# Kernel optimization log

Measured on AMD Instinct MI355X. Metric: run time of the kernel, lower is better.

The kernel has to match this reference:

```python
import jax, jax.numpy as jnp
import numpy as np

P = 7       # patch (window) size
H_HEADS = 8
D_HEAD = 64
SCALE = D_HEAD ** -0.5


def setup_inputs() -> dict:
    key = jax.random.key(0)
    k1, k2, k3, k4 = jax.random.split(key, 4)
    dim, inner = 256, H_HEADS * D_HEAD
    fmap = jax.random.normal(k1, (32, 56, 56, dim), dtype=jnp.float32)
    Wq = jax.random.normal(k2, (dim, inner), dtype=jnp.float32) * (dim ** -0.5)
    Wkv = jax.random.normal(k3, (dim, 2 * inner), dtype=jnp.float32) * (dim ** -0.5)
    Wo = jax.random.normal(k4, (inner, dim), dtype=jnp.float32) * (inner ** -0.5)
    bo = jnp.zeros((dim,), dtype=jnp.float32)
    return {"fmap": fmap, "Wq": Wq, "Wkv": Wkv, "Wo": Wo, "bo": bo}


def reference(fmap, Wq, Wkv, Wo, bo):
    b, X, Y, c = fmap.shape
    x, y = X // P, Y // P
    h, d = H_HEADS, D_HEAD
    # window partition: b (x p1) (y p2) c -> (b x y) p1 p2 c
    f = fmap.reshape(b, x, P, y, P, c).transpose(0, 1, 3, 2, 4, 5)
    f = f.reshape(b * x * y, P, P, c)
    # 1x1 convs == matmul over channels
    q = f @ Wq                       # (B, p, p, h*d)
    k_, v = jnp.split(f @ Wkv, 2, axis=-1)
    B = b * x * y
    pp = P * P
    def to_heads(t):  # (B,p,p,h*d) -> (B,h,pp,d)
        return t.reshape(B, pp, h, d).transpose(0, 2, 1, 3)
    q, k_, v = map(to_heads, (q, k_, v))
    dots = jnp.einsum('bhid,bhjd->bhij', q, k_) * SCALE
    attn = jax.nn.softmax(dots, axis=-1)
    out = jnp.einsum('bhij,bhjd->bhid', attn, v)      # (B,h,pp,d)
    # (b x y h) (p1 p2) d -> b (x p1) (y p2) (h d)
    out = out.reshape(b, x, y, h, P, P, d)
    out = out.transpose(0, 1, 4, 2, 5, 3, 6).reshape(b, X, Y, h * d)
    return out @ Wo + bo
```

## Files before the change

kernel.cpp:

```cpp
#include <hip/hip_runtime.h>
#include <hip/hip_bf16.h>

typedef __bf16 bf16;
typedef __bf16 bf16x4 __attribute__((ext_vector_type(4)));
typedef __bf16 bf16x8 __attribute__((ext_vector_type(8)));
typedef float f32x4 __attribute__((ext_vector_type(4)));

#define TOK 100352
#define ATT_SCALE 0.125f

#define GLOAD_LDS16(g, l)                                                        \
  __builtin_amdgcn_global_load_lds((const __attribute__((address_space(1))) void*)(g), \
                                   (__attribute__((address_space(3))) void*)(l), 16, 0, 0)

__global__ __launch_bounds__(256) void transpose_cast_k(const float* __restrict__ in,
                                                        bf16* __restrict__ out, int R, int C) {
  __shared__ float t[32][33];
  int c0 = blockIdx.x * 32, r0 = blockIdx.y * 32;
  int tx = threadIdx.x, ty = threadIdx.y;
#pragma unroll
  for (int i = ty; i < 32; i += 8)
    t[i][tx] = in[(size_t)(r0 + i) * C + c0 + tx];
  __syncthreads();
#pragma unroll
  for (int i = ty; i < 32; i += 8)
    out[(size_t)(c0 + i) * R + r0 + tx] = (bf16)t[tx][i];
}

__global__ __launch_bounds__(256) void cast_partition_k(const float* __restrict__ fmap,
                                                        bf16* __restrict__ A, int tok0) {
  int tid = blockIdx.x * 256 + threadIdx.x;
  int tokl = tid >> 5, cg = (tid & 31) << 3;
  int tok = tok0 + tokl;
  int w = tok / 49, t = tok - w * 49;
  int p1 = t / 7, p2 = t - p1 * 7;
  int bb = w >> 6, xx = (w >> 3) & 7, yy = w & 7;
  size_t src = ((((size_t)bb * 56) + xx * 7 + p1) * 56 + yy * 7 + p2) * 256 + cg;
  float4 f0 = *(const float4*)(fmap + src);
  float4 f1 = *(const float4*)(fmap + src + 4);
  bf16x8 o;
  o[0] = (bf16)f0.x; o[1] = (bf16)f0.y; o[2] = (bf16)f0.z; o[3] = (bf16)f0.w;
  o[4] = (bf16)f1.x; o[5] = (bf16)f1.y; o[6] = (bf16)f1.z; o[7] = (bf16)f1.w;
  *(bf16x8*)(A + (size_t)tokl * 256 + cg) = o;
}

template <int KD, int ND, int EPI>
__global__ __launch_bounds__(256) void gemm_bt_k(const bf16* __restrict__ A,
                                                 const bf16* __restrict__ Bt,
                                                 bf16* __restrict__ Cb, float* __restrict__ Cf,
                                                 const float* __restrict__ bias, int tok0) {
  __shared__ bf16 As[128 * 64], Bs[128 * 64];
  const int tid = threadIdx.x;
  const int lane = tid & 63, wv = tid >> 6;
  const int l15 = lane & 15, l4 = lane >> 4;
  const int bn = blockIdx.x, bm = blockIdx.y;
  const int mb = (wv >> 1) * 64, nb = (wv & 1) * 64;
  const int srow = wv * 32 + (lane >> 3);
  const int scol = ((lane & 7) ^ ((lane >> 3) & 7)) * 8;
  const bf16* Ab = A + (size_t)(bm * 128 + srow) * KD + scol;
  const bf16* Bb = Bt + (size_t)(bn * 128 + srow) * KD + scol;
  f32x4 acc[4][4] = {};
  for (int ks = 0; ks < KD / 64; ++ks) {
#pragma unroll
    for (int i = 0; i < 4; ++i) {
      GLOAD_LDS16(Ab + (size_t)i * 8 * KD + ks * 64, As + wv * 2048 + i * 512);
      GLOAD_LDS16(Bb + (size_t)i * 8 * KD + ks * 64, Bs + wv * 2048 + i * 512);
    }
    __syncthreads();
#pragma unroll
    for (int kk = 0; kk < 2; ++kk) {
      bf16x8 af[4], bfr[4];
#pragma unroll
      for (int m = 0; m < 4; ++m) {
        int r = mb + m * 16 + l15;
        af[m] = *(const bf16x8*)((const char*)As +
                 ((r * 128 + kk * 64 + l4 * 16) ^ ((r & 7) << 4)));
      }
#pragma unroll
      for (int n = 0; n < 4; ++n) {
        int r = nb + n * 16 + l15;
        bfr[n] = *(const bf16x8*)((const char*)Bs +
                 ((r * 128 + kk * 64 + l4 * 16) ^ ((r & 7) << 4)));
      }
#pragma unroll
      for (int m = 0; m < 4; ++m)
#pragma unroll
        for (int n = 0; n < 4; ++n)
          acc[m][n] = __builtin_amdgcn_mfma_f32_16x16x32_bf16(bfr[n], af[m], acc[m][n], 0, 0, 0);
    }
    __syncthreads();
  }
  if constexpr (EPI == 1) {
#pragma unroll
    for (int m = 0; m < 4; ++m) {
      size_t row = (size_t)bm * 128 + mb + m * 16 + l15;
#pragma unroll
      for (int n = 0; n < 4; ++n) {
        int col = bn * 128 + nb + n * 16 + l4 * 4;
        bf16x4 pk;
#pragma unroll
        for (int r = 0; r < 4; ++r) pk[r] = (bf16)acc[m][n][r];
        *(bf16x4*)(Cb + row * ND + col) = pk;
      }
    }
  } else {
#pragma unroll
    for (int m = 0; m < 4; ++m) {
      int tok = tok0 + bm * 128 + mb + m * 16 + l15;
      int w = tok / 49, t = tok - w * 49;
      int p1 = t / 7, p2 = t - p1 * 7;
      int bb = w >> 6, xx = (w >> 3) & 7, yy = w & 7;
      size_t orow = (((size_t)bb * 56) + xx * 7 + p1) * 56 + yy * 7 + p2;
#pragma unroll
      for (int n = 0; n < 4; ++n) {
        int col = bn * 128 + nb + n * 16 + l4 * 4;
        float4 b4 = *(const float4*)(bias + col);
        float4 v;
        v.x = acc[m][n][0] + b4.x;
        v.y = acc[m][n][1] + b4.y;
        v.z = acc[m][n][2] + b4.z;
        v.w = acc[m][n][3] + b4.w;
        *(float4*)(Cf + orow * 256 + col) = v;
      }
    }
  }
}

__global__ __launch_bounds__(256) void attn_win_k(const bf16* __restrict__ qkv,
                                                  bf16* __restrict__ attn) {
  __shared__ bf16 Qs[64 * 64], Ks[64 * 64], Vt[64 * 64], Ps[4 * 16 * 64];
  int blk = blockIdx.x;
  int w = blk >> 3, h = blk & 7;
  int tid = threadIdx.x, lane = tid & 63, wv = tid >> 6;
  int l15 = lane & 15, l4 = lane >> 4;
  const size_t base = (size_t)w * 49 * 1536 + h * 64;
#pragma unroll
  for (int i = 0; i < 2; ++i) {
    int j = i * 256 + tid, r = j >> 3, cc = j & 7;
    int off = (r * 128 + cc * 16) ^ ((r & 7) << 4);
    uint4 zq = {0, 0, 0, 0}, zk = {0, 0, 0, 0};
    if (r < 49) {
      zq = *(const uint4*)(qkv + base + (size_t)r * 1536 + cc * 8);
      zk = *(const uint4*)(qkv + base + 512 + (size_t)r * 1536 + cc * 8);
    }
    *(uint4*)((char*)Qs + off) = zq;
    *(uint4*)((char*)Ks + off) = zk;
  }
#pragma unroll
  for (int i = 0; i < 2; ++i) {
    int j = i * 256 + tid, r = j >> 3, cg = j & 7;
    if (r < 49) {
      uint4 v = *(const uint4*)(qkv + base + 1024 + (size_t)r * 1536 + cg * 8);
      const bf16* pv = (const bf16*)&v;
#pragma unroll
      for (int e = 0; e < 8; ++e) {
        int c = cg * 8 + e;
        int off = ((c * 64 + r) * 2) ^ (((c >> 3) & 7) << 4);
        *(bf16*)((char*)Vt + off) = pv[e];
      }
    } else {
#pragma unroll
      for (int e = 0; e < 8; ++e) {
        int c = cg * 8 + e;
        int off = ((c * 64 + r) * 2) ^ (((c >> 3) & 7) << 4);
        *(bf16*)((char*)Vt + off) = (bf16)0.0f;
      }
    }
  }
  __syncthreads();
  f32x4 s[4] = {};
#pragma unroll
  for (int kk = 0; kk < 2; ++kk) {
    int rq = wv * 16 + l15;
    bf16x8 aq = *(const bf16x8*)((const char*)Qs +
                ((rq * 128 + kk * 64 + l4 * 16) ^ ((rq & 7) << 4)));
#pragma unroll
    for (int n = 0; n < 4; ++n) {
      int rk = n * 16 + l15;
      bf16x8 bk = *(const bf16x8*)((const char*)Ks +
                  ((rk * 128 + kk * 64 + l4 * 16) ^ ((rk & 7) << 4)));
      s[n] = __builtin_amdgcn_mfma_f32_16x16x32_bf16(aq, bk, s[n], 0, 0, 0);
    }
  }
  float pr[4][4];
#pragma unroll
  for (int reg = 0; reg < 4; ++reg) {
    float m = -1e30f;
#pragma unroll
    for (int n = 0; n < 4; ++n) {
      float v = s[n][reg] * ATT_SCALE;
      if (n * 16 + l15 < 49) m = fmaxf(m, v);
    }
#pragma unroll
    for (int d = 1; d < 16; d <<= 1) m = fmaxf(m, __shfl_xor(m, d));
    float sum = 0.f;
#pragma unroll
    for (int n = 0; n < 4; ++n) {
      float p = (n * 16 + l15 < 49) ? __expf(s[n][reg] * ATT_SCALE - m) : 0.f;
      pr[n][reg] = p;
      sum += p;
    }
#pragma unroll
    for (int d = 1; d < 16; d <<= 1) sum += __shfl_xor(sum, d);
    float inv = 1.f / sum;
#pragma unroll
    for (int n = 0; n < 4; ++n) pr[n][reg] *= inv;
  }
  char* pbase = (char*)Ps + wv * 2048;
#pragma unroll
  for (int n = 0; n < 4; ++n)
#pragma unroll
    for (int reg = 0; reg < 4; ++reg) {
      int rl = l4 * 4 + reg, col = n * 16 + l15;
      int off = ((rl * 64 + col) * 2) ^ ((rl & 7) << 4);
      *(bf16*)(pbase + off) = (bf16)pr[n][reg];
    }
  __syncthreads();
  f32x4 o[4] = {};
#pragma unroll
  for (int kk = 0; kk < 2; ++kk) {
    int rp = l15;
    bf16x8 ap = *(const bf16x8*)(pbase +
                ((rp * 128 + kk * 64 + l4 * 16) ^ ((rp & 7) << 4)));
#pragma unroll
    for (int n = 0; n < 4; ++n) {
      int rv = n * 16 + l15;
      bf16x8 bv = *(const bf16x8*)((const char*)Vt +
                  ((rv * 128 + kk * 64 + l4 * 16) ^ (((rv >> 3) & 7) << 4)));
      o[n] = __builtin_amdgcn_mfma_f32_16x16x32_bf16(bv, ap, o[n], 0, 0, 0);
    }
  }
  int rl = wv * 16 + l15;
  if (rl < 49) {
    size_t rowoff = ((size_t)w * 49 + rl) * 512 + h * 64;
#pragma unroll
    for (int n = 0; n < 4; ++n) {
      bf16x4 pk;
#pragma unroll
      for (int r = 0; r < 4; ++r) pk[r] = (bf16)o[n][r];
      *(bf16x4*)(attn + rowoff + n * 16 + l4 * 4) = pk;
    }
  }
}

extern "C" void kernel_launch(void* const* d_in, const int* in_sizes, int n_in,
                              void* d_out, int out_size, void* d_ws, size_t ws_size,
                              hipStream_t stream) {
  const float* fmap = (const float*)d_in[0];
  const float* Wq = (const float*)d_in[1];
  const float* Wkv = (const float*)d_in[2];
  const float* Wo = (const float*)d_in[3];
  const float* bo = (const float*)d_in[4];
  float* out = (float*)d_out;
  char* ws = (char*)d_ws;

  const size_t WQKV_B = 1536ull * 256 * 2;
  const size_t WO_B = 256ull * 512 * 2;
  const size_t wbytes = WQKV_B + WO_B;

  int nc = 0;
  size_t Tc = 0;
  for (int c = 1; c <= 16; c <<= 1) {
    size_t tc = TOK / c;
    if (wbytes + tc * 4608ull <= ws_size) { nc = c; Tc = tc; break; }
  }
  if (nc == 0) return;

  bf16* Wqkv_t = (bf16*)(ws);
  bf16* Wo_t = (bf16*)(ws + WQKV_B);
  bf16* Abuf = (bf16*)(ws + wbytes);
  bf16* qkv = (bf16*)(ws + wbytes + Tc * 512);
  bf16* attn = (bf16*)(ws + wbytes + Tc * 512 + Tc * 3072);

  hipLaunchKernelGGL(transpose_cast_k, dim3(16, 8), dim3(32, 8), 0, stream, Wq, Wqkv_t, 256, 512);
  hipLaunchKernelGGL(transpose_cast_k, dim3(32, 8), dim3(32, 8), 0, stream, Wkv,
                     Wqkv_t + 512 * 256, 256, 1024);
  hipLaunchKernelGGL(transpose_cast_k, dim3(8, 16), dim3(32, 8), 0, stream, Wo, Wo_t, 512, 256);

  for (int c = 0; c < nc; ++c) {
    int tok0 = (int)(c * Tc);
    int wloc = (int)(Tc / 49);
    hipLaunchKernelGGL(cast_partition_k, dim3((int)(Tc / 8)), dim3(256), 0, stream, fmap, Abuf,
                       tok0);
    hipLaunchKernelGGL((gemm_bt_k<256, 1536, 1>), dim3(12, (int)(Tc / 128)), dim3(256), 0, stream,
                       Abuf, Wqkv_t, qkv, nullptr, nullptr, 0);
    hipLaunchKernelGGL(attn_win_k, dim3(wloc * 8), dim3(256), 0, stream, qkv, attn);
    hipLaunchKernelGGL((gemm_bt_k<512, 256, 2>), dim3(2, (int)(Tc / 128)), dim3(256), 0, stream,
                       attn, Wo_t, nullptr, out, bo, tok0);
  }
}
```

Baseline: 366.5 us.

## Fuse window partition into QKV GEMM and output projection into attention

Result: slower. 426.1 us (+16.3%).

```diff
diff --git a/kernel.cpp b/kernel.cpp
--- a/kernel.cpp
+++ b/kernel.cpp
@@ -27,28 +27,9 @@
     out[(size_t)(c0 + i) * R + r0 + tx] = (bf16)t[tx][i];
 }
 
-__global__ __launch_bounds__(256) void cast_partition_k(const float* __restrict__ fmap,
-                                                        bf16* __restrict__ A, int tok0) {
-  int tid = blockIdx.x * 256 + threadIdx.x;
-  int tokl = tid >> 5, cg = (tid & 31) << 3;
-  int tok = tok0 + tokl;
-  int w = tok / 49, t = tok - w * 49;
-  int p1 = t / 7, p2 = t - p1 * 7;
-  int bb = w >> 6, xx = (w >> 3) & 7, yy = w & 7;
-  size_t src = ((((size_t)bb * 56) + xx * 7 + p1) * 56 + yy * 7 + p2) * 256 + cg;
-  float4 f0 = *(const float4*)(fmap + src);
-  float4 f1 = *(const float4*)(fmap + src + 4);
-  bf16x8 o;
-  o[0] = (bf16)f0.x; o[1] = (bf16)f0.y; o[2] = (bf16)f0.z; o[3] = (bf16)f0.w;
-  o[4] = (bf16)f1.x; o[5] = (bf16)f1.y; o[6] = (bf16)f1.z; o[7] = (bf16)f1.w;
-  *(bf16x8*)(A + (size_t)tokl * 256 + cg) = o;
-}
-
-template <int KD, int ND, int EPI>
-__global__ __launch_bounds__(256) void gemm_bt_k(const bf16* __restrict__ A,
-                                                 const bf16* __restrict__ Bt,
-                                                 bf16* __restrict__ Cb, float* __restrict__ Cf,
-                                                 const float* __restrict__ bias, int tok0) {
+__global__ __launch_bounds__(256) void qkv_gemm_k(const float* __restrict__ fmap,
+                                                  const bf16* __restrict__ Bt,
+                                                  bf16* __restrict__ Cb, int tok0) {
   __shared__ bf16 As[128 * 64], Bs[128 * 64];
   const int tid = threadIdx.x;
   const int lane = tid & 63, wv = tid >> 6;
@@ -57,14 +38,33 @@
   const int mb = (wv >> 1) * 64, nb = (wv & 1) * 64;
   const int srow = wv * 32 + (lane >> 3);
   const int scol = ((lane & 7) ^ ((lane >> 3) & 7)) * 8;
-  const bf16* Ab = A + (size_t)(bm * 128 + srow) * KD + scol;
-  const bf16* Bb = Bt + (size_t)(bn * 128 + srow) * KD + scol;
+  const bf16* Bb = Bt + (size_t)(bn * 128 + srow) * 256 + scol;
+  const int arow = tid >> 3;
+  const int acc8 = tid & 7;
+  int sro[4];
+#pragma unroll
+  for (int i = 0; i < 4; ++i) {
+    int tok = tok0 + bm * 128 + i * 32 + arow;
+    int w = tok / 49, t = tok - w * 49;
+    int p1 = t / 7, p2 = t - p1 * 7;
+    int bb = w >> 6, xx = (w >> 3) & 7, yy = w & 7;
+    sro[i] = ((bb * 56 + xx * 7 + p1) * 56 + yy * 7 + p2) * 256;
+  }
   f32x4 acc[4][4] = {};
-  for (int ks = 0; ks < KD / 64; ++ks) {
+  for (int ks = 0; ks < 4; ++ks) {
+#pragma unroll
+    for (int i = 0; i < 4; ++i)
+      GLOAD_LDS16(Bb + (size_t)i * 8 * 256 + ks * 64, Bs + wv * 2048 + i * 512);
 #pragma unroll
     for (int i = 0; i < 4; ++i) {
-      GLOAD_LDS16(Ab + (size_t)i * 8 * KD + ks * 64, As + wv * 2048 + i * 512);
-      GLOAD_LDS16(Bb + (size_t)i * 8 * KD + ks * 64, Bs + wv * 2048 + i * 512);
+      const float* p = fmap + sro[i] + ks * 64 + acc8 * 8;
+      float4 f0 = *(const float4*)p;
+      float4 f1 = *(const float4*)(p + 4);
+      bf16x8 o;
+      o[0] = (bf16)f0.x; o[1] = (bf16)f0.y; o[2] = (bf16)f0.z; o[3] = (bf16)f0.w;
+      o[4] = (bf16)f1.x; o[5] = (bf16)f1.y; o[6] = (bf16)f1.z; o[7] = (bf16)f1.w;
+      int r = i * 32 + arow;
+      *(bf16x8*)((char*)As + ((r * 128 + acc8 * 16) ^ ((r & 7) << 4))) = o;
     }
     __syncthreads();
 #pragma unroll
@@ -90,67 +90,51 @@
     }
     __syncthreads();
   }
-  if constexpr (EPI == 1) {
-#pragma unroll
-    for (int m = 0; m < 4; ++m) {
-      size_t row = (size_t)bm * 128 + mb + m * 16 + l15;
-#pragma unroll
-      for (int n = 0; n < 4; ++n) {
-        int col = bn * 128 + nb + n * 16 + l4 * 4;
-        bf16x4 pk;
-#pragma unroll
-        for (int r = 0; r < 4; ++r) pk[r] = (bf16)acc[m][n][r];
-        *(bf16x4*)(Cb + row * ND + col) = pk;
-      }
-    }
-  } else {
-#pragma unroll
-    for (int m = 0; m < 4; ++m) {
-      int tok = tok0 + bm * 128 + mb + m * 16 + l15;
-      int w = tok / 49, t = tok - w * 49;
-      int p1 = t / 7, p2 = t - p1 * 7;
-      int bb = w >> 6, xx = (w >> 3) & 7, yy = w & 7;
-      size_t orow = (((size_t)bb * 56) + xx * 7 + p1) * 56 + yy * 7 + p2;
-#pragma unroll
-      for (int n = 0; n < 4; ++n) {
-        int col = bn * 128 + nb + n * 16 + l4 * 4;
-        float4 b4 = *(const float4*)(bias + col);
-        float4 v;
-        v.x = acc[m][n][0] + b4.x;
-        v.y = acc[m][n][1] + b4.y;
-        v.z = acc[m][n][2] + b4.z;
-        v.w = acc[m][n][3] + b4.w;
-        *(float4*)(Cf + orow * 256 + col) = v;
-      }
+#pragma unroll
+  for (int m = 0; m < 4; ++m) {
+    size_t row = (size_t)bm * 128 + mb + m * 16 + l15;
+#pragma unroll
+    for (int n = 0; n < 4; ++n) {
+      int col = bn * 128 + nb + n * 16 + l4 * 4;
+      bf16x4 pk;
+#pragma unroll
+      for (int r = 0; r < 4; ++r) pk[r] = (bf16)acc[m][n][r];
+      *(bf16x4*)(Cb + row * 1536 + col) = pk;
     }
   }
 }
 
-__global__ __launch_bounds__(256) void attn_win_k(const bf16* __restrict__ qkv,
-                                                  bf16* __restrict__ attn) {
-  __shared__ bf16 Qs[64 * 64], Ks[64 * 64], Vt[64 * 64], Ps[4 * 16 * 64];
-  int blk = blockIdx.x;
-  int w = blk >> 3, h = blk & 7;
-  int tid = threadIdx.x, lane = tid & 63, wv = tid >> 6;
-  int l15 = lane & 15, l4 = lane >> 4;
-  const size_t base = (size_t)w * 49 * 1536 + h * 64;
-#pragma unroll
-  for (int i = 0; i < 2; ++i) {
-    int j = i * 256 + tid, r = j >> 3, cc = j & 7;
-    int off = (r * 128 + cc * 16) ^ ((r & 7) << 4);
-    uint4 zq = {0, 0, 0, 0}, zk = {0, 0, 0, 0};
-    if (r < 49) {
-      zq = *(const uint4*)(qkv + base + (size_t)r * 1536 + cc * 8);
-      zk = *(const uint4*)(qkv + base + 512 + (size_t)r * 1536 + cc * 8);
-    }
-    *(uint4*)((char*)Qs + off) = zq;
-    *(uint4*)((char*)Ks + off) = zk;
-  }
-#pragma unroll
-  for (int i = 0; i < 2; ++i) {
-    int j = i * 256 + tid, r = j >> 3, cg = j & 7;
-    if (r < 49) {
-      uint4 v = *(const uint4*)(qkv + base + 1024 + (size_t)r * 1536 + cg * 8);
+__global__ __launch_bounds__(256) void attn_fused_k(const bf16* __restrict__ qkv,
+                                                    const bf16* __restrict__ Wo_t,
+                                                    const float* __restrict__ bias,
+                                                    float* __restrict__ out, int wbase) {
+  __shared__ bf16 Qs[64 * 64], Ks[64 * 64], Vt[64 * 64], Ps[4 * 16 * 64], HO[64 * 64];
+  const int w = blockIdx.x;
+  const int tid = threadIdx.x, lane = tid & 63, wv = tid >> 6;
+  const int l15 = lane & 15, l4 = lane >> 4;
+  const size_t base = (size_t)w * 49 * 1536;
+  const int wg = wbase + w;
+  char* pbase = (char*)Ps + wv * 2048;
+  f32x4 acco[4][4] = {};
+  for (int h = 0; h < 8; ++h) {
+    const size_t hb = base + h * 64;
+#pragma unroll
+    for (int i = 0; i < 2; ++i) {
+      int j = i * 256 + tid, r = j >> 3, cc = j & 7;
+      int off = (r * 128 + cc * 16) ^ ((r & 7) << 4);
+      uint4 zq = {0, 0, 0, 0}, zk = {0, 0, 0, 0};
+      if (r < 49) {
+        zq = *(const uint4*)(qkv + hb + (size_t)r * 1536 + cc * 8);
+        zk = *(const uint4*)(qkv + hb + 512 + (size_t)r * 1536 + cc * 8);
+      }
+      *(uint4*)((char*)Qs + off) = zq;
+      *(uint4*)((char*)Ks + off) = zk;
+    }
+#pragma unroll
+    for (int i = 0; i < 2; ++i) {
+      int j = i * 256 + tid, r = j >> 3, cg = j & 7;
+      uint4 v = {0, 0, 0, 0};
+      if (r < 49) v = *(const uint4*)(qkv + hb + 1024 + (size_t)r * 1536 + cg * 8);
       const bf16* pv = (const bf16*)&v;
 #pragma unroll
       for (int e = 0; e < 8; ++e) {
@@ -158,87 +142,118 @@
         int off = ((c * 64 + r) * 2) ^ (((c >> 3) & 7) << 4);
         *(bf16*)((char*)Vt + off) = pv[e];
       }
-    } else {
-#pragma unroll
-      for (int e = 0; e < 8; ++e) {
-        int c = cg * 8 + e;
-        int off = ((c * 64 + r) * 2) ^ (((c >> 3) & 7) << 4);
-        *(bf16*)((char*)Vt + off) = (bf16)0.0f;
-      }
-    }
-  }
-  __syncthreads();
-  f32x4 s[4] = {};
-#pragma unroll
-  for (int kk = 0; kk < 2; ++kk) {
-    int rq = wv * 16 + l15;
-    bf16x8 aq = *(const bf16x8*)((const char*)Qs +
-                ((rq * 128 + kk * 64 + l4 * 16) ^ ((rq & 7) << 4)));
-#pragma unroll
-    for (int n = 0; n < 4; ++n) {
-      int rk = n * 16 + l15;
-      bf16x8 bk = *(const bf16x8*)((const char*)Ks +
-                  ((rk * 128 + kk * 64 + l4 * 16) ^ ((rk & 7) << 4)));
-      s[n] = __builtin_amdgcn_mfma_f32_16x16x32_bf16(aq, bk, s[n], 0, 0, 0);
-    }
-  }
-  float pr[4][4];
-#pragma unroll
-  for (int reg = 0; reg < 4; ++reg) {
-    float m = -1e30f;
-#pragma unroll
-    for (int n = 0; n < 4; ++n) {
-      float v = s[n][reg] * ATT_SCALE;
-      if (n * 16 + l15 < 49) m = fmaxf(m, v);
-    }
-#pragma unroll
-    for (int d = 1; d < 16; d <<= 1) m = fmaxf(m, __shfl_xor(m, d));
-    float sum = 0.f;
-#pragma unroll
-    for (int n = 0; n < 4; ++n) {
-      float p = (n * 16 + l15 < 49) ? __expf(s[n][reg] * ATT_SCALE - m) : 0.f;
-      pr[n][reg] = p;
-      sum += p;
-    }
-#pragma unroll
-    for (int d = 1; d < 16; d <<= 1) sum += __shfl_xor(sum, d);
-    float inv = 1.f / sum;
-#pragma unroll
-    for (int n = 0; n < 4; ++n) pr[n][reg] *= inv;
-  }
-  char* pbase = (char*)Ps + wv * 2048;
-#pragma unroll
-  for (int n = 0; n < 4; ++n)
+    }
+    __syncthreads();
+    f32x4 s[4] = {};
+#pragma unroll
+    for (int kk = 0; kk < 2; ++kk) {
+      int rq = wv * 16 + l15;
+      bf16x8 aq = *(const bf16x8*)((const char*)Qs +
+                  ((rq * 128 + kk * 64 + l4 * 16) ^ ((rq & 7) << 4)));
+#pragma unroll
+      for (int n = 0; n < 4; ++n) {
+        int rk = n * 16 + l15;
+        bf16x8 bk = *(const bf16x8*)((const char*)Ks +
+                    ((rk * 128 + kk * 64 + l4 * 16) ^ ((rk & 7) << 4)));
+        s[n] = __builtin_amdgcn_mfma_f32_16x16x32_bf16(aq, bk, s[n], 0, 0, 0);
+      }
+    }
+    float pr[4][4];
 #pragma unroll
     for (int reg = 0; reg < 4; ++reg) {
-      int rl = l4 * 4 + reg, col = n * 16 + l15;
-      int off = ((rl * 64 + col) * 2) ^ ((rl & 7) << 4);
-      *(bf16*)(pbase + off) = (bf16)pr[n][reg];
-    }
-  __syncthreads();
-  f32x4 o[4] = {};
-#pragma unroll
-  for (int kk = 0; kk < 2; ++kk) {
-    int rp = l15;
-    bf16x8 ap = *(const bf16x8*)(pbase +
-                ((rp * 128 + kk * 64 + l4 * 16) ^ ((rp & 7) << 4)));
-#pragma unroll
-    for (int n = 0; n < 4; ++n) {
-      int rv = n * 16 + l15;
-      bf16x8 bv = *(const bf16x8*)((const char*)Vt +
-                  ((rv * 128 + kk * 64 + l4 * 16) ^ (((rv >> 3) & 7) << 4)));
-      o[n] = __builtin_amdgcn_mfma_f32_16x16x32_bf16(bv, ap, o[n], 0, 0, 0);
-    }
-  }
-  int rl = wv * 16 + l15;
-  if (rl < 49) {
-    size_t rowoff = ((size_t)w * 49 + rl) * 512 + h * 64;
-#pragma unroll
-    for (int n = 0; n < 4; ++n) {
-      bf16x4 pk;
-#pragma unroll
-      for (int r = 0; r < 4; ++r) pk[r] = (bf16)o[n][r];
-      *(bf16x4*)(attn + rowoff + n * 16 + l4 * 4) = pk;
+      float m = -1e30f;
+#pragma unroll
+      for (int n = 0; n < 4; ++n) {
+        float v = s[n][reg] * ATT_SCALE;
+        if (n * 16 + l15 < 49) m = fmaxf(m, v);
+      }
+#pragma unroll
+      for (int d = 1; d < 16; d <<= 1) m = fmaxf(m, __shfl_xor(m, d));
+      float sum = 0.f;
+#pragma unroll
+      for (int n = 0; n < 4; ++n) {
+        float p = (n * 16 + l15 < 49) ? __expf(s[n][reg] * ATT_SCALE - m) : 0.f;
+        pr[n][reg] = p;
+        sum += p;
+      }
+#pragma unroll
+      for (int d = 1; d < 16; d <<= 1) sum += __shfl_xor(sum, d);
+      float inv = 1.f / sum;
+#pragma unroll
+      for (int n = 0; n < 4; ++n) pr[n][reg] *= inv;
+    }
+#pragma unroll
+    for (int n = 0; n < 4; ++n)
+#pragma unroll
+      for (int reg = 0; reg < 4; ++reg) {
+        int rl = l4 * 4 + reg, col = n * 16 + l15;
+        int off = ((rl * 64 + col) * 2) ^ ((rl & 7) << 4);
+        *(bf16*)(pbase + off) = (bf16)pr[n][reg];
+      }
+    f32x4 o[4] = {};
+#pragma unroll
+    for (int kk = 0; kk < 2; ++kk) {
+      int rp = l15;
+      bf16x8 ap = *(const bf16x8*)(pbase +
+                  ((rp * 128 + kk * 64 + l4 * 16) ^ ((rp & 7) << 4)));
+#pragma unroll
+      for (int n = 0; n < 4; ++n) {
+        int rv = n * 16 + l15;
+        bf16x8 bv = *(const bf16x8*)((const char*)Vt +
+                    ((rv * 128 + kk * 64 + l4 * 16) ^ (((rv >> 3) & 7) << 4)));
+        o[n] = __builtin_amdgcn_mfma_f32_16x16x32_bf16(bv, ap, o[n], 0, 0, 0);
+      }
+    }
+    {
+      int hrow = wv * 16 + l15;
+#pragma unroll
+      for (int n = 0; n < 4; ++n) {
+        bf16x4 pk;
+#pragma unroll
+        for (int r = 0; r < 4; ++r) pk[r] = (bf16)o[n][r];
+        int off = (hrow * 128 + n * 32 + l4 * 8) ^ ((hrow & 7) << 4);
+        *(bf16x4*)((char*)HO + off) = pk;
+      }
+    }
+    __syncthreads();
+#pragma unroll
+    for (int kk = 0; kk < 2; ++kk) {
+      bf16x8 af[4];
+#pragma unroll
+      for (int m = 0; m < 4; ++m) {
+        int r = m * 16 + l15;
+        af[m] = *(const bf16x8*)((const char*)HO +
+                 ((r * 128 + kk * 64 + l4 * 16) ^ ((r & 7) << 4)));
+      }
+#pragma unroll
+      for (int n = 0; n < 4; ++n) {
+        int wr = wv * 64 + n * 16 + l15;
+        bf16x8 bv = *(const bf16x8*)(Wo_t + (size_t)wr * 512 + h * 64 + kk * 32 + l4 * 8);
+#pragma unroll
+        for (int m = 0; m < 4; ++m)
+          acco[m][n] = __builtin_amdgcn_mfma_f32_16x16x32_bf16(bv, af[m], acco[m][n], 0, 0, 0);
+      }
+    }
+  }
+  int bb = wg >> 6, xx = (wg >> 3) & 7, yy = wg & 7;
+#pragma unroll
+  for (int m = 0; m < 4; ++m) {
+    int rl = m * 16 + l15;
+    if (rl < 49) {
+      int p1 = rl / 7, p2 = rl - p1 * 7;
+      size_t orow = (size_t)(bb * 56 + xx * 7 + p1) * 56 + yy * 7 + p2;
+      float* op = out + orow * 256 + wv * 64;
+#pragma unroll
+      for (int n = 0; n < 4; ++n) {
+        int col = n * 16 + l4 * 4;
+        float4 b4 = *(const float4*)(bias + wv * 64 + col);
+        float4 v;
+        v.x = acco[m][n][0] + b4.x;
+        v.y = acco[m][n][1] + b4.y;
+        v.z = acco[m][n][2] + b4.z;
+        v.w = acco[m][n][3] + b4.w;
+        *(float4*)(op + col) = v;
+      }
     }
   }
 }
@@ -260,17 +275,15 @@
 
   int nc = 0;
   size_t Tc = 0;
-  for (int c = 1; c <= 16; c <<= 1) {
+  for (int c = 2; c <= 16; c <<= 1) {
     size_t tc = TOK / c;
-    if (wbytes + tc * 4608ull <= ws_size) { nc = c; Tc = tc; break; }
+    if (wbytes + tc * 3072ull <= ws_size) { nc = c; Tc = tc; break; }
   }
   if (nc == 0) return;
 
   bf16* Wqkv_t = (bf16*)(ws);
   bf16* Wo_t = (bf16*)(ws + WQKV_B);
-  bf16* Abuf = (bf16*)(ws + wbytes);
-  bf16* qkv = (bf16*)(ws + wbytes + Tc * 512);
-  bf16* attn = (bf16*)(ws + wbytes + Tc * 512 + Tc * 3072);
+  bf16* qkv = (bf16*)(ws + wbytes);
 
   hipLaunchKernelGGL(transpose_cast_k, dim3(16, 8), dim3(32, 8), 0, stream, Wq, Wqkv_t, 256, 512);
   hipLaunchKernelGGL(transpose_cast_k, dim3(32, 8), dim3(32, 8), 0, stream, Wkv,
@@ -279,13 +292,9 @@
 
   for (int c = 0; c < nc; ++c) {
     int tok0 = (int)(c * Tc);
-    int wloc = (int)(Tc / 49);
-    hipLaunchKernelGGL(cast_partition_k, dim3((int)(Tc / 8)), dim3(256), 0, stream, fmap, Abuf,
-                       tok0);
-    hipLaunchKernelGGL((gemm_bt_k<256, 1536, 1>), dim3(12, (int)(Tc / 128)), dim3(256), 0, stream,
-                       Abuf, Wqkv_t, qkv, nullptr, nullptr, 0);
-    hipLaunchKernelGGL(attn_win_k, dim3(wloc * 8), dim3(256), 0, stream, qkv, attn);
-    hipLaunchKernelGGL((gemm_bt_k<512, 256, 2>), dim3(2, (int)(Tc / 128)), dim3(256), 0, stream,
-                       attn, Wo_t, nullptr, out, bo, tok0);
+    hipLaunchKernelGGL(qkv_gemm_k, dim3(12, (int)(Tc / 128)), dim3(256), 0, stream, fmap, Wqkv_t,
+                       qkv, tok0);
+    hipLaunchKernelGGL(attn_fused_k, dim3((int)(Tc / 49)), dim3(256), 0, stream, qkv, Wo_t, bo,
+                       out, tok0 / 49);
   }
 }
```
